# Optimization experiments

Hardware: AMD Instinct MI355X
Metric: run time of the kernel (lower is better)

The kernel has to match this reference:

```python
import jax, jax.numpy as jnp
import numpy as np

B, T, D = 2, 1024, 2048
H, HKV, DH = 16, 4, 128
G = H // HKV  # GQA groups
F = 5632
ROPE_THETA = 10000.0
EPS = 1e-6


def _rope_tables(t, dh, theta):
    inv = 1.0 / (theta ** (np.arange(0, dh, 2, dtype=np.float32) / dh))  # [dh//2]
    ang = np.outer(np.arange(t, dtype=np.float32), inv)                  # [T, dh//2]
    return jnp.asarray(np.cos(ang)), jnp.asarray(np.sin(ang))


def setup_inputs() -> dict:
    key = jax.random.key(0)
    ks = jax.random.split(key, 9)
    s = 0.02
    cos, sin = _rope_tables(T, DH, ROPE_THETA)
    return {
        "x": jax.random.normal(ks[0], (B, T, D), jnp.float32),
        "freqs_cos": cos,
        "freqs_sin": sin,
        "w_norm1": jnp.ones((D,), jnp.float32),
        "w_norm2": jnp.ones((D,), jnp.float32),
        "wq": jax.random.normal(ks[1], (D, H * DH), jnp.float32) * s,
        "wk": jax.random.normal(ks[2], (D, HKV * DH), jnp.float32) * s,
        "wv": jax.random.normal(ks[3], (D, HKV * DH), jnp.float32) * s,
        "wo": jax.random.normal(ks[4], (D, D), jnp.float32) * s,
        "w1": jax.random.normal(ks[5], (D, F), jnp.float32) * s,
        "w2": jax.random.normal(ks[6], (F, D), jnp.float32) * s,
        "w3": jax.random.normal(ks[7], (D, F), jnp.float32) * s,
    }


def _rmsnorm(x, w):
    var = jnp.mean(jnp.square(x), axis=-1, keepdims=True)
    return x * jax.lax.rsqrt(var + EPS) * w


def _apply_rope(x, cos, sin):
    # x: [B, T, nH, DH]; cos/sin: [T, DH//2]
    xr = x.reshape(*x.shape[:-1], DH // 2, 2)
    x0, x1 = xr[..., 0], xr[..., 1]
    c = cos[None, :, None, :]
    s = sin[None, :, None, :]
    o0 = x0 * c - x1 * s
    o1 = x0 * s + x1 * c
    return jnp.stack([o0, o1], axis=-1).reshape(x.shape)


def reference(x, freqs_cos, freqs_sin, w_norm1, w_norm2, wq, wk, wv, wo, w1, w2, w3):
    residual = x
    xn = _rmsnorm(x, w_norm1)
    q = (xn @ wq).reshape(B, T, H, DH)
    k = (xn @ wk).reshape(B, T, HKV, DH)
    v = (xn @ wv).reshape(B, T, HKV, DH)
    q = _apply_rope(q, freqs_cos, freqs_sin)
    k = _apply_rope(k, freqs_cos, freqs_sin)
    # grouped heads: q -> [B, HKV, G, T, DH]; k,v -> [B, HKV, T, DH]
    q = q.transpose(0, 2, 1, 3).reshape(B, HKV, G, T, DH)
    k = k.transpose(0, 2, 1, 3)
    v = v.transpose(0, 2, 1, 3)
    scale = DH ** -0.5
    scores = jnp.einsum("bkgtd,bksd->bkgts", q, k) * scale  # [B,HKV,G,T,T]
    causal = jnp.tril(jnp.ones((T, T), dtype=bool))
    scores = jnp.where(causal, scores, -jnp.inf)
    attn = jax.nn.softmax(scores, axis=-1)
    out = jnp.einsum("bkgts,bksd->bkgtd", attn, v)  # [B,HKV,G,T,DH]
    out = out.reshape(B, H, T, DH).transpose(0, 2, 1, 3).reshape(B, T, D)
    x = residual + out @ wo
    h = _rmsnorm(x, w_norm2)
    ffn = (jax.nn.silu(h @ w1) * (h @ w3)) @ w2
    return x + ffn
```

## Files before the change

### kernel.cpp

```cpp
#include <hip/hip_runtime.h>
#include <hip/hip_bf16.h>
#include <math.h>

typedef __hip_bfloat16 bf16;
typedef __attribute__((ext_vector_type(8))) short bf16x8;
typedef __attribute__((ext_vector_type(4))) float f32x4;

__device__ __forceinline__ float b2f(bf16 v) { return __bfloat162float(v); }
__device__ __forceinline__ bf16  f2b(float v) { return __float2bfloat16(v); }

constexpr int Bc = 2, Tc = 1024, Dc = 2048, Hc = 16, HKVc = 4, DHc = 128, Fc = 5632;
constexpr int Mr = Bc * Tc;
constexpr int Nqkv = Hc * DHc + 2 * HKVc * DHc;

__device__ __forceinline__ void g2l16(void* lds, const void* g) {
  __builtin_amdgcn_global_load_lds(
      (const __attribute__((address_space(1))) unsigned int*)g,
      (__attribute__((address_space(3))) unsigned int*)lds, 16, 0, 0);
}

__global__ __launch_bounds__(256) void tcast_k(const float* __restrict__ src,
                                               bf16* __restrict__ dst,
                                               int N, int K) {
  __shared__ bf16 tile[64][68];
  const int t = threadIdx.x;
  const int n0 = blockIdx.x * 64, k0 = blockIdx.y * 64;
#pragma unroll
  for (int it = 0; it < 4; ++it) {
    const int kl = it * 16 + (t >> 4);
    const int nl = (t & 15) * 4;
    float4 v = *reinterpret_cast<const float4*>(src + (size_t)(k0 + kl) * N + n0 + nl);
    tile[kl][nl]     = f2b(v.x);
    tile[kl][nl + 1] = f2b(v.y);
    tile[kl][nl + 2] = f2b(v.z);
    tile[kl][nl + 3] = f2b(v.w);
  }
  __syncthreads();
  union { uint4 u; bf16 h[8]; } o;
#pragma unroll
  for (int it = 0; it < 2; ++it) {
    const int nl = it * 32 + (t >> 3);
    const int kl = (t & 7) * 8;
#pragma unroll
    for (int j = 0; j < 8; ++j) o.h[j] = tile[kl + j][nl];
    *reinterpret_cast<uint4*>(dst + (size_t)(n0 + nl) * K + k0 + kl) = o.u;
  }
}

__global__ __launch_bounds__(256) void tcast_ffn(const float* __restrict__ src,
                                                 bf16* __restrict__ dst,
                                                 int off) {
  __shared__ bf16 tile[64][68];
  const int t = threadIdx.x;
  const int n0 = blockIdx.x * 64, k0 = blockIdx.y * 64;
#pragma unroll
  for (int it = 0; it < 4; ++it) {
    const int kl = it * 16 + (t >> 4);
    const int nl = (t & 15) * 4;
    float4 v = *reinterpret_cast<const float4*>(src + (size_t)(k0 + kl) * Fc + n0 + nl);
    tile[kl][nl]     = f2b(v.x);
    tile[kl][nl + 1] = f2b(v.y);
    tile[kl][nl + 2] = f2b(v.z);
    tile[kl][nl + 3] = f2b(v.w);
  }
  __syncthreads();
  union { uint4 u; bf16 h[8]; } o;
#pragma unroll
  for (int it = 0; it < 2; ++it) {
    const int nl = it * 32 + (t >> 3);
    const int kl = (t & 7) * 8;
#pragma unroll
    for (int j = 0; j < 8; ++j) o.h[j] = tile[kl + j][nl];
    const int n = n0 + nl;
    const int r = ((n >> 4) << 5) + (n & 15) + off;
    *reinterpret_cast<uint4*>(dst + (size_t)r * Dc + k0 + kl) = o.u;
  }
}

__global__ __launch_bounds__(256) void rmsnorm_k(const float* __restrict__ x,
                                                 const float* __restrict__ w,
                                                 bf16* __restrict__ out) {
  const size_t rbase = (size_t)blockIdx.x * Dc;
  float ss = 0.f;
  for (int i = threadIdx.x; i < Dc; i += 256) {
    float v = x[rbase + i];
    ss += v * v;
  }
#pragma unroll
  for (int off = 32; off > 0; off >>= 1) ss += __shfl_down(ss, off, 64);
  __shared__ float red[4];
  const int lane = threadIdx.x & 63, wid = threadIdx.x >> 6;
  if (lane == 0) red[wid] = ss;
  __syncthreads();
  const float scale = rsqrtf((red[0] + red[1] + red[2] + red[3]) / (float)Dc + 1e-6f);
  for (int i = threadIdx.x; i < Dc; i += 256)
    out[rbase + i] = f2b(x[rbase + i] * scale * w[i]);
}

template <bool ADDRES>
__global__ __launch_bounds__(256) void gemm128(const bf16* __restrict__ A,
                                               const bf16* __restrict__ Bt,
                                               const float* __restrict__ Res,
                                               void* __restrict__ Out,
                                               int N, int K) {
  __shared__ __align__(16) bf16 As[128 * 32];
  __shared__ __align__(16) bf16 Bs[128 * 32];
  const int t = threadIdx.x;
  const int bm = blockIdx.y * 128, bn = blockIdx.x * 128;
  const int lane = t & 63, wv = t >> 6;
  const int wm = (wv & 1) * 64, wn = (wv >> 1) * 64;
  const int sr = t >> 2, sc = (t & 3) * 8;
  const bf16* ga = A + (size_t)(bm + sr) * K + sc;
  const bf16* gb = Bt + (size_t)(bn + sr) * K + sc;
  bf16* lA0 = As + sr * 32 + sc;
  bf16* lA1 = As + (64 + sr) * 32 + sc;
  bf16* lB0 = Bs + sr * 32 + sc;
  bf16* lB1 = Bs + (64 + sr) * 32 + sc;
  const size_t rstep = (size_t)64 * K;
  f32x4 acc[4][4] = {};
  const int fr = lane & 15, fko = (lane >> 4) * 8;
  for (int k0 = 0; k0 < K; k0 += 32) {
    __syncthreads();
    g2l16(lA0, ga + k0);
    g2l16(lA1, ga + rstep + k0);
    g2l16(lB0, gb + k0);
    g2l16(lB1, gb + rstep + k0);
    __syncthreads();
    bf16x8 af[4], bff[4];
#pragma unroll
    for (int i = 0; i < 4; ++i)
      af[i] = *reinterpret_cast<const bf16x8*>(As + (wm + i * 16 + fr) * 32 + fko);
#pragma unroll
    for (int j = 0; j < 4; ++j)
      bff[j] = *reinterpret_cast<const bf16x8*>(Bs + (wn + j * 16 + fr) * 32 + fko);
#pragma unroll
    for (int i = 0; i < 4; ++i)
#pragma unroll
      for (int j = 0; j < 4; ++j)
        acc[i][j] = __builtin_amdgcn_mfma_f32_16x16x32_bf16(af[i], bff[j], acc[i][j], 0, 0, 0);
  }
  const int er = (lane >> 4) * 4, ec = lane & 15;
#pragma unroll
  for (int i = 0; i < 4; ++i)
#pragma unroll
    for (int j = 0; j < 4; ++j) {
      const int row = bm + wm + i * 16 + er;
      const int col = bn + wn + j * 16 + ec;
#pragma unroll
      for (int r = 0; r < 4; ++r) {
        const size_t idx = (size_t)(row + r) * N + col;
        if (ADDRES) ((float*)Out)[idx] = Res[idx] + acc[i][j][r];
        else        ((bf16*)Out)[idx] = f2b(acc[i][j][r]);
      }
    }
}

template <int K>
__global__ __launch_bounds__(512, 2) void ffn_gemm256(const bf16* __restrict__ A,
                                                      const bf16* __restrict__ B,
                                                      bf16* __restrict__ act) {
  constexpr int NT = K / 64;
  constexpr int NIT = NT / 2;
  __shared__ bf16 As[2 * 256 * 64];
  __shared__ bf16 Bs[3 * 256 * 64];
  const int tid = threadIdx.x;
  const int lane = tid & 63, wv = tid >> 6;
  const int wr = wv >> 2, wc = wv & 3;
  const int fr = lane & 15, quad = lane >> 4;
  const int swz = fr & 7;
  const int bm = blockIdx.y * 256;
  const int bn = blockIdx.x * 256;
  const int lrow = tid >> 3;
  const int scol = ((tid & 7) ^ (lrow & 7)) * 8;
  const size_t rstep = (size_t)64 * K;

  auto stageA = [&](int t, int half) {
    const int buf = (t & 1) * 16384;
    const bf16* g = A + (size_t)(bm + half * 128 + lrow) * K + t * 64 + scol;
    bf16* d = As + buf + half * 8192 + (size_t)tid * 8;
    g2l16(d, g);
    g2l16(d + 4096, g + rstep);
  };
  auto stageB = [&](int t, int half, int buf) {
    const bf16* g = B + (size_t)(bn + half * 128 + lrow) * K + t * 64 + scol;
    bf16* d = Bs + buf * 16384 + half * 8192 + (size_t)tid * 8;
    g2l16(d, g);
    g2l16(d + 4096, g + rstep);
  };

  f32x4 acc[8][4] = {};
  const int u0 = (quad ^ swz) * 8;

  stageA(0, 0); stageA(0, 1);
  stageB(0, 0, 0); stageB(0, 1, 0);
  stageB(1, 0, 1); stageB(1, 1, 1);
  asm volatile("s_waitcnt vmcnt(4)" ::: "memory");
  __builtin_amdgcn_s_barrier();

  int rb0 = 0, rb1 = 1, sb = 2;
  for (int it = 0; it < NIT; ++it) {
    const int t1 = 2 * it + 1;
#pragma unroll
    for (int j = 0; j < 8; ++j) {
      const int bufT = (j < 4) ? 0 : 16384;
      const int bufB = ((j < 4) ? rb0 : rb1) * 16384;
      const int qr4 = ((j & 3) >> 1) * 4, qc2 = ((j & 3) & 1) * 2;
      bf16x8 af[4][2], bv[2][2];
      const bf16* Ab = As + bufT + (size_t)(wr * 128 + fr) * 64;
      const bf16* Bb = Bs + bufB + (size_t)(wc * 64 + fr) * 64;
#pragma unroll
      for (int ii = 0; ii < 4; ++ii) {
        af[ii][0] = *reinterpret_cast<const bf16x8*>(Ab + (qr4 + ii) * 1024 + u0);
        af[ii][1] = *reinterpret_cast<const bf16x8*>(Ab + (qr4 + ii) * 1024 + (u0 ^ 32));
      }
#pragma unroll
      for (int jj = 0; jj < 2; ++jj) {
        bv[jj][0] = *reinterpret_cast<const bf16x8*>(Bb + (qc2 + jj) * 1024 + u0);
        bv[jj][1] = *reinterpret_cast<const bf16x8*>(Bb + (qc2 + jj) * 1024 + (u0 ^ 32));
      }
      if (j == 0)      stageA(t1, 0);
      else if (j == 1) stageA(t1, 1);
      else if (j == 2) { if (2 * it + 2 < NT) stageB(2 * it + 2, 0, sb); }
      else if (j == 3) { if (2 * it + 2 < NT) stageB(2 * it + 2, 1, sb); }
      else if (j == 4) { if (2 * it + 2 < NT) stageA(2 * it + 2, 0); }
      else if (j == 5) { if (2 * it + 2 < NT) stageA(2 * it + 2, 1); }
      else if (j == 6) { if (2 * it + 3 < NT) stageB(2 * it + 3, 0, rb0); }
      else             { if (2 * it + 3 < NT) stageB(2 * it + 3, 1, rb0); }
      __builtin_amdgcn_s_barrier();
      asm volatile("s_waitcnt lgkmcnt(0)" ::: "memory");
      __builtin_amdgcn_sched_barrier(0);
      __builtin_amdgcn_s_setprio(1);
#pragma unroll
      for (int ii = 0; ii < 4; ++ii)
#pragma unroll
        for (int jj = 0; jj < 2; ++jj) {
          acc[qr4 + ii][qc2 + jj] = __builtin_amdgcn_mfma_f32_16x16x32_bf16(
              af[ii][0], bv[jj][0], acc[qr4 + ii][qc2 + jj], 0, 0, 0);
          acc[qr4 + ii][qc2 + jj] = __builtin_amdgcn_mfma_f32_16x16x32_bf16(
              af[ii][1], bv[jj][1], acc[qr4 + ii][qc2 + jj], 0, 0, 0);
        }
      __builtin_amdgcn_s_setprio(0);
      if (j == 3) {
        if (2 * it + 2 < NT) asm volatile("s_waitcnt vmcnt(4)" ::: "memory");
        else                 asm volatile("s_waitcnt vmcnt(0)" ::: "memory");
      } else if (j == 7) {
        if (2 * it + 3 < NT)      asm volatile("s_waitcnt vmcnt(4)" ::: "memory");
        else if (2 * it + 2 < NT) asm volatile("s_waitcnt vmcnt(0)" ::: "memory");
      }
      __builtin_amdgcn_s_barrier();
    }
    const int nrb0 = sb; sb = rb1; rb1 = rb0; rb0 = nrb0;
  }

  const int er = quad * 4, ec = lane & 15;
#pragma unroll
  for (int i = 0; i < 8; ++i) {
    const int row = bm + wr * 128 + i * 16 + er;
#pragma unroll
    for (int jp = 0; jp < 2; ++jp) {
      const f32x4 g = acc[i][2 * jp], u = acc[i][2 * jp + 1];
      const int f = blockIdx.x * 128 + wc * 32 + jp * 16 + ec;
#pragma unroll
      for (int r = 0; r < 4; ++r) {
        const float sg = g[r] / (1.f + __expf(-g[r]));
        act[(size_t)(row + r) * Fc + f] = f2b(sg * u[r]);
      }
    }
  }
}

__global__ __launch_bounds__(256) void repack_k(const bf16* __restrict__ qkv,
                                                const float* __restrict__ cosb,
                                                const float* __restrict__ sinb,
                                                bf16* __restrict__ Qr,
                                                bf16* __restrict__ Kr,
                                                bf16* __restrict__ Vt) {
  const int bt = blockIdx.x;
  const int b = bt >> 10, tp = bt & (Tc - 1);
  const int t0 = threadIdx.x;
  const bf16* row = qkv + (size_t)bt * Nqkv;
#pragma unroll
  for (int k = 0; k < 4; ++k) {
    int p2 = k * 256 + t0;
    int hh = p2 >> 6, i = p2 & 63;
    float c = cosb[tp * 64 + i], sn = sinb[tp * 64 + i];
    float x0 = b2f(row[hh * 128 + 2 * i]), x1 = b2f(row[hh * 128 + 2 * i + 1]);
    bf16* dst = Qr + ((size_t)(b * Hc + hh) * Tc + tp) * DHc + 2 * i;
    dst[0] = f2b(x0 * c - x1 * sn);
    dst[1] = f2b(x0 * sn + x1 * c);
  }
  {
    int hh = t0 >> 6, i = t0 & 63;
    float c = cosb[tp * 64 + i], sn = sinb[tp * 64 + i];
    float x0 = b2f(row[2048 + hh * 128 + 2 * i]), x1 = b2f(row[2048 + hh * 128 + 2 * i + 1]);
    bf16* dst = Kr + ((size_t)(b * HKVc + hh) * Tc + tp) * DHc + 2 * i;
    dst[0] = f2b(x0 * c - x1 * sn);
    dst[1] = f2b(x0 * sn + x1 * c);
  }
#pragma unroll
  for (int k = 0; k < 2; ++k) {
    int e = k * 256 + t0;
    int kvh = e >> 7, dd = e & 127;
    Vt[((size_t)(b * HKVc + kvh) * DHc + dd) * Tc + tp] = row[2560 + e];
  }
}

__global__ __launch_bounds__(256) void fattn(const bf16* __restrict__ Qr,
                                             const bf16* __restrict__ Kr,
                                             const bf16* __restrict__ Vt,
                                             bf16* __restrict__ ao) {
  __shared__ __align__(16) bf16 Ks[64 * 136];
  __shared__ __align__(16) bf16 Vts[128 * 72];
  __shared__ __align__(16) bf16 Ps[4][16 * 72];
  const int idx = blockIdx.x;
  const int r = idx & 15;
  const int qt = (r & 1) ? (15 - (r >> 1)) : (r >> 1);
  const int h = (idx >> 4) & 15;
  const int b = idx >> 8;
  const int kv = h >> 2;
  const int t = threadIdx.x, lane = t & 63, wv = t >> 6;
  const int fr = lane & 15, quad = lane >> 4;

  const bf16* Qbase = Qr + ((size_t)(b * Hc + h) * Tc + qt * 64) * DHc;
  const bf16* Kbase = Kr + (size_t)(b * HKVc + kv) * Tc * DHc;
  const bf16* Vbase = Vt + (size_t)(b * HKVc + kv) * DHc * Tc;

  bf16x8 qf[4];
#pragma unroll
  for (int c = 0; c < 4; ++c)
    qf[c] = *reinterpret_cast<const bf16x8*>(Qbase + (size_t)(wv * 16 + fr) * DHc + c * 32 + quad * 8);

  float m[4], l[4];
  f32x4 o[8] = {};
#pragma unroll
  for (int r2 = 0; r2 < 4; ++r2) { m[r2] = -3.0e38f; l[r2] = 0.f; }

  for (int kt = 0; kt <= qt; ++kt) {
    __syncthreads();
    {
      const bf16* src = Kbase + (size_t)kt * 64 * DHc;
#pragma unroll
      for (int i2 = 0; i2 < 4; ++i2) {
        int flat = i2 * 256 + t;
        int row = flat >> 4, c16 = flat & 15;
        uint4 v = *reinterpret_cast<const uint4*>(src + (size_t)row * DHc + c16 * 8);
        *reinterpret_cast<uint4*>(&Ks[row * 136 + c16 * 8]) = v;
      }
#pragma unroll
      for (int i2 = 0; i2 < 4; ++i2) {
        int flat = i2 * 256 + t;
        int row = flat >> 3, c8 = flat & 7;
        uint4 v = *reinterpret_cast<const uint4*>(Vbase + (size_t)row * Tc + kt * 64 + c8 * 8);
        *reinterpret_cast<uint4*>(&Vts[row * 72 + c8 * 8]) = v;
      }
    }
    __syncthreads();
    f32x4 s[4];
#pragma unroll
    for (int cb = 0; cb < 4; ++cb) {
      f32x4 acc = {};
#pragma unroll
      for (int kc = 0; kc < 4; ++kc) {
        bf16x8 kf = *reinterpret_cast<const bf16x8*>(&Ks[(cb * 16 + fr) * 136 + kc * 32 + quad * 8]);
        acc = __builtin_amdgcn_mfma_f32_16x16x32_bf16(qf[kc], kf, acc, 0, 0, 0);
      }
      s[cb] = acc * 0.08838834764831845f;
    }
    if (kt == qt) {
#pragma unroll
      for (int cb = 0; cb < 4; ++cb)
#pragma unroll
        for (int r2 = 0; r2 < 4; ++r2) {
          int key = cb * 16 + fr;
          int qg = wv * 16 + quad * 4 + r2;
          if (key > qg) s[cb][r2] = -3.0e38f;
        }
    }
    float tm[4], ts[4];
#pragma unroll
    for (int r2 = 0; r2 < 4; ++r2)
      tm[r2] = fmaxf(fmaxf(s[0][r2], s[1][r2]), fmaxf(s[2][r2], s[3][r2]));
#pragma unroll
    for (int off = 1; off < 16; off <<= 1)
#pragma unroll
      for (int r2 = 0; r2 < 4; ++r2)
        tm[r2] = fmaxf(tm[r2], __shfl_xor(tm[r2], off, 64));
    float al[4];
#pragma unroll
    for (int r2 = 0; r2 < 4; ++r2) {
      float mn = fmaxf(m[r2], tm[r2]);
      al[r2] = __expf(m[r2] - mn);
      m[r2] = mn;
      ts[r2] = 0.f;
    }
#pragma unroll
    for (int cb = 0; cb < 4; ++cb)
#pragma unroll
      for (int r2 = 0; r2 < 4; ++r2) {
        float e = __expf(s[cb][r2] - m[r2]);
        s[cb][r2] = e;
        ts[r2] += e;
      }
#pragma unroll
    for (int off = 1; off < 16; off <<= 1)
#pragma unroll
      for (int r2 = 0; r2 < 4; ++r2)
        ts[r2] += __shfl_xor(ts[r2], off, 64);
#pragma unroll
    for (int r2 = 0; r2 < 4; ++r2) l[r2] = l[r2] * al[r2] + ts[r2];
#pragma unroll
    for (int db = 0; db < 8; ++db)
#pragma unroll
      for (int r2 = 0; r2 < 4; ++r2) o[db][r2] *= al[r2];
    bf16* pw = Ps[wv];
#pragma unroll
    for (int cb = 0; cb < 4; ++cb)
#pragma unroll
      for (int r2 = 0; r2 < 4; ++r2)
        pw[(quad * 4 + r2) * 72 + cb * 16 + fr] = f2b(s[cb][r2]);
    bf16x8 pa[2];
    pa[0] = *reinterpret_cast<const bf16x8*>(&pw[fr * 72 + quad * 8]);
    pa[1] = *reinterpret_cast<const bf16x8*>(&pw[fr * 72 + 32 + quad * 8]);
#pragma unroll
    for (int db = 0; db < 8; ++db) {
      bf16x8 v0 = *reinterpret_cast<const bf16x8*>(&Vts[(db * 16 + fr) * 72 + quad * 8]);
      bf16x8 v1 = *reinterpret_cast<const bf16x8*>(&Vts[(db * 16 + fr) * 72 + 32 + quad * 8]);
      o[db] = __builtin_amdgcn_mfma_f32_16x16x32_bf16(pa[0], v0, o[db], 0, 0, 0);
      o[db] = __builtin_amdgcn_mfma_f32_16x16x32_bf16(pa[1], v1, o[db], 0, 0, 0);
    }
  }
#pragma unroll
  for (int r2 = 0; r2 < 4; ++r2) {
    float inv = 1.f / l[r2];
    int qg = qt * 64 + wv * 16 + quad * 4 + r2;
    bf16* orow = ao + (size_t)(b * Tc + qg) * Dc + h * DHc;
#pragma unroll
    for (int db = 0; db < 8; ++db)
      orow[db * 16 + fr] = f2b(o[db][r2] * inv);
  }
}

extern "C" void kernel_launch(void* const* d_in, const int* in_sizes, int n_in,
                              void* d_out, int out_size, void* d_ws, size_t ws_size,
                              hipStream_t stream) {
  const float* x    = (const float*)d_in[0];
  const float* fcos = (const float*)d_in[1];
  const float* fsin = (const float*)d_in[2];
  const float* wn1  = (const float*)d_in[3];
  const float* wn2  = (const float*)d_in[4];
  const float* wq   = (const float*)d_in[5];
  const float* wk   = (const float*)d_in[6];
  const float* wv   = (const float*)d_in[7];
  const float* wo   = (const float*)d_in[8];
  const float* w1   = (const float*)d_in[9];
  const float* w2   = (const float*)d_in[10];
  const float* w3   = (const float*)d_in[11];

  char* p = (char*)d_ws;
  bf16* wqkv_t = (bf16*)p;                 p += (size_t)Nqkv * Dc * 2;
  bf16* qkv    = (bf16*)p;                 p += (size_t)Mr * Nqkv * 2;
  float* xat   = (float*)d_ws;
  bf16* wo_t = (bf16*)p;                   p += (size_t)Dc * Dc * 2;
  bf16* w13t = (bf16*)p;                   p += (size_t)2 * Fc * Dc * 2;
  bf16* w2t  = w13t;
  bf16* xn   = (bf16*)p;                   p += (size_t)Mr * Dc * 2;
  bf16* ao   = (bf16*)p;                   p += (size_t)Mr * Dc * 2;
  bf16* act  = (bf16*)p;                   p += (size_t)Mr * Fc * 2;
  bf16* hb = xn;
  bf16* Qr = act;
  bf16* Kr = act + (size_t)Mr * Hc * DHc;
  bf16* Vtb = Kr + (size_t)Mr * HKVc * DHc;

  const dim3 blk(256);
  tcast_k<<<dim3(32, 32), blk, 0, stream>>>(wq, wqkv_t, 2048, 2048);
  tcast_k<<<dim3(8, 32), blk, 0, stream>>>(wk, wqkv_t + (size_t)2048 * 2048, 512, 2048);
  tcast_k<<<dim3(8, 32), blk, 0, stream>>>(wv, wqkv_t + (size_t)2560 * 2048, 512, 2048);
  tcast_k<<<dim3(32, 32), blk, 0, stream>>>(wo, wo_t, 2048, 2048);
  tcast_ffn<<<dim3(88, 32), blk, 0, stream>>>(w1, w13t, 0);
  tcast_ffn<<<dim3(88, 32), blk, 0, stream>>>(w3, w13t, 16);

  rmsnorm_k<<<Mr, blk, 0, stream>>>(x, wn1, xn);
  gemm128<false><<<dim3(Nqkv / 128, Mr / 128), blk, 0, stream>>>(xn, wqkv_t, nullptr, qkv, Nqkv, Dc);
  repack_k<<<Mr, blk, 0, stream>>>(qkv, fcos, fsin, Qr, Kr, Vtb);
  fattn<<<Bc * Hc * 16, blk, 0, stream>>>(Qr, Kr, Vtb, ao);
  gemm128<true><<<dim3(Dc / 128, Mr / 128), blk, 0, stream>>>(ao, wo_t, x, xat, Dc, Dc);
  rmsnorm_k<<<Mr, blk, 0, stream>>>(xat, wn2, hb);
  ffn_gemm256<Dc><<<dim3(2 * Fc / 256, Mr / 256), dim3(512), 0, stream>>>(hb, w13t, act);
  tcast_k<<<dim3(32, 88), blk, 0, stream>>>(w2, w2t, 2048, 5632);
  gemm128<true><<<dim3(Dc / 128, Mr / 128), blk, 0, stream>>>(act, w2t, xat, (float*)d_out, Dc, Fc);
}
```

Before: 645.1 us.

## Use split-K 256-tile GEMM with atomic accumulation for Wo and W2 projections

Replaces the 128-tile residual GEMMs for the output projection and the FFN down projection with a 256x256 tile, 512-thread kernel that splits K four ways and accumulates into an output prefilled with the residual via float atomics. A copy kernel seeds the output with the residual first. This is meant to raise the number of blocks for the small 2048x2048 outputs (64 tiles to 256 blocks) and use a deeper, more efficient pipelined MFMA loop. It adds an extra full-tensor copy, atomic traffic, and nondeterministic summation order.

New measurement: 653.2 us. No clear change (+1.3%).

```diff
diff --git a/kernel.cpp b/kernel.cpp
--- a/kernel.cpp
+++ b/kernel.cpp
@@ -75,6 +75,12 @@
     const int r = ((n >> 4) << 5) + (n & 15) + off;
     *reinterpret_cast<uint4*>(dst + (size_t)r * Dc + k0 + kl) = o.u;
   }
+}
+
+__global__ __launch_bounds__(256) void copy_f32(const float* __restrict__ src,
+                                                float* __restrict__ dst) {
+  const int i = blockIdx.x * 256 + threadIdx.x;
+  reinterpret_cast<float4*>(dst)[i] = reinterpret_cast<const float4*>(src)[i];
 }
 
 __global__ __launch_bounds__(256) void rmsnorm_k(const float* __restrict__ x,
@@ -269,6 +275,119 @@
   }
 }
 
+template <int KFULL, int KSUB>
+__global__ __launch_bounds__(512, 2) void gemm256sk(const bf16* __restrict__ A,
+                                                    const bf16* __restrict__ Bt,
+                                                    float* __restrict__ Out,
+                                                    int N) {
+  constexpr int NT = KSUB / 64;
+  constexpr int NIT = NT / 2;
+  __shared__ bf16 As[2 * 256 * 64];
+  __shared__ bf16 Bs[3 * 256 * 64];
+  const int tid = threadIdx.x;
+  const int lane = tid & 63, wv = tid >> 6;
+  const int wr = wv >> 2, wc = wv & 3;
+  const int fr = lane & 15, quad = lane >> 4;
+  const int swz = fr & 7;
+  const int bm = blockIdx.y * 256;
+  const int bn = blockIdx.x * 256;
+  const int kbase = blockIdx.z * KSUB;
+  const int lrow = tid >> 3;
+  const int scol = ((tid & 7) ^ (lrow & 7)) * 8;
+  const size_t rstep = (size_t)64 * KFULL;
+
+  auto stageA = [&](int t, int half) {
+    const int buf = (t & 1) * 16384;
+    const bf16* g = A + (size_t)(bm + half * 128 + lrow) * KFULL + kbase + t * 64 + scol;
+    bf16* d = As + buf + half * 8192 + (size_t)tid * 8;
+    g2l16(d, g);
+    g2l16(d + 4096, g + rstep);
+  };
+  auto stageB = [&](int t, int half, int buf) {
+    const bf16* g = Bt + (size_t)(bn + half * 128 + lrow) * KFULL + kbase + t * 64 + scol;
+    bf16* d = Bs + buf * 16384 + half * 8192 + (size_t)tid * 8;
+    g2l16(d, g);
+    g2l16(d + 4096, g + rstep);
+  };
+
+  f32x4 acc[8][4] = {};
+  const int u0 = (quad ^ swz) * 8;
+
+  stageA(0, 0); stageA(0, 1);
+  stageB(0, 0, 0); stageB(0, 1, 0);
+  stageB(1, 0, 1); stageB(1, 1, 1);
+  asm volatile("s_waitcnt vmcnt(4)" ::: "memory");
+  __builtin_amdgcn_s_barrier();
+
+  int rb0 = 0, rb1 = 1, sb = 2;
+  for (int it = 0; it < NIT; ++it) {
+    const int t1 = 2 * it + 1;
+#pragma unroll
+    for (int j = 0; j < 8; ++j) {
+      const int bufT = (j < 4) ? 0 : 16384;
+      const int bufB = ((j < 4) ? rb0 : rb1) * 16384;
+      const int qr4 = ((j & 3) >> 1) * 4, qc2 = ((j & 3) & 1) * 2;
+      bf16x8 af[4][2], bv[2][2];
+      const bf16* Ab = As + bufT + (size_t)(wr * 128 + fr) * 64;
+      const bf16* Bb = Bs + bufB + (size_t)(wc * 64 + fr) * 64;
+#pragma unroll
+      for (int ii = 0; ii < 4; ++ii) {
+        af[ii][0] = *reinterpret_cast<const bf16x8*>(Ab + (qr4 + ii) * 1024 + u0);
+        af[ii][1] = *reinterpret_cast<const bf16x8*>(Ab + (qr4 + ii) * 1024 + (u0 ^ 32));
+      }
+#pragma unroll
+      for (int jj = 0; jj < 2; ++jj) {
+        bv[jj][0] = *reinterpret_cast<const bf16x8*>(Bb + (qc2 + jj) * 1024 + u0);
+        bv[jj][1] = *reinterpret_cast<const bf16x8*>(Bb + (qc2 + jj) * 1024 + (u0 ^ 32));
+      }
+      if (j == 0)      stageA(t1, 0);
+      else if (j == 1) stageA(t1, 1);
+      else if (j == 2) { if (2 * it + 2 < NT) stageB(2 * it + 2, 0, sb); }
+      else if (j == 3) { if (2 * it + 2 < NT) stageB(2 * it + 2, 1, sb); }
+      else if (j == 4) { if (2 * it + 2 < NT) stageA(2 * it + 2, 0); }
+      else if (j == 5) { if (2 * it + 2 < NT) stageA(2 * it + 2, 1); }
+      else if (j == 6) { if (2 * it + 3 < NT) stageB(2 * it + 3, 0, rb0); }
+      else             { if (2 * it + 3 < NT) stageB(2 * it + 3, 1, rb0); }
+      __builtin_amdgcn_s_barrier();
+      asm volatile("s_waitcnt lgkmcnt(0)" ::: "memory");
+      __builtin_amdgcn_sched_barrier(0);
+      __builtin_amdgcn_s_setprio(1);
+#pragma unroll
+      for (int ii = 0; ii < 4; ++ii)
+#pragma unroll
+        for (int jj = 0; jj < 2; ++jj) {
+          acc[qr4 + ii][qc2 + jj] = __builtin_amdgcn_mfma_f32_16x16x32_bf16(
+              af[ii][0], bv[jj][0], acc[qr4 + ii][qc2 + jj], 0, 0, 0);
+          acc[qr4 + ii][qc2 + jj] = __builtin_amdgcn_mfma_f32_16x16x32_bf16(
+              af[ii][1], bv[jj][1], acc[qr4 + ii][qc2 + jj], 0, 0, 0);
+        }
+      __builtin_amdgcn_s_setprio(0);
+      if (j == 3) {
+        if (2 * it + 2 < NT) asm volatile("s_waitcnt vmcnt(4)" ::: "memory");
+        else                 asm volatile("s_waitcnt vmcnt(0)" ::: "memory");
+      } else if (j == 7) {
+        if (2 * it + 3 < NT)      asm volatile("s_waitcnt vmcnt(4)" ::: "memory");
+        else if (2 * it + 2 < NT) asm volatile("s_waitcnt vmcnt(0)" ::: "memory");
+      }
+      __builtin_amdgcn_s_barrier();
+    }
+    const int nrb0 = sb; sb = rb1; rb1 = rb0; rb0 = nrb0;
+  }
+
+  const int er = quad * 4, ec = lane & 15;
+#pragma unroll
+  for (int i = 0; i < 8; ++i) {
+    const int row = bm + wr * 128 + i * 16 + er;
+#pragma unroll
+    for (int jc = 0; jc < 4; ++jc) {
+      const int col = bn + wc * 64 + jc * 16 + ec;
+#pragma unroll
+      for (int r = 0; r < 4; ++r)
+        atomicAdd(&Out[(size_t)(row + r) * N + col], acc[i][jc][r]);
+    }
+  }
+}
+
 __global__ __launch_bounds__(256) void repack_k(const bf16* __restrict__ qkv,
                                                 const float* __restrict__ cosb,
                                                 const float* __restrict__ sinb,
@@ -483,9 +602,11 @@
   gemm128<false><<<dim3(Nqkv / 128, Mr / 128), blk, 0, stream>>>(xn, wqkv_t, nullptr, qkv, Nqkv, Dc);
   repack_k<<<Mr, blk, 0, stream>>>(qkv, fcos, fsin, Qr, Kr, Vtb);
   fattn<<<Bc * Hc * 16, blk, 0, stream>>>(Qr, Kr, Vtb, ao);
-  gemm128<true><<<dim3(Dc / 128, Mr / 128), blk, 0, stream>>>(ao, wo_t, x, xat, Dc, Dc);
+  copy_f32<<<Mr * Dc / 1024, blk, 0, stream>>>(x, xat);
+  gemm256sk<Dc, 512><<<dim3(Dc / 256, Mr / 256, 4), dim3(512), 0, stream>>>(ao, wo_t, xat, Dc);
   rmsnorm_k<<<Mr, blk, 0, stream>>>(xat, wn2, hb);
   ffn_gemm256<Dc><<<dim3(2 * Fc / 256, Mr / 256), dim3(512), 0, stream>>>(hb, w13t, act);
   tcast_k<<<dim3(32, 88), blk, 0, stream>>>(w2, w2t, 2048, 5632);
-  gemm128<true><<<dim3(Dc / 128, Mr / 128), blk, 0, stream>>>(act, w2t, xat, (float*)d_out, Dc, Fc);
-}
+  copy_f32<<<Mr * Dc / 1024, blk, 0, stream>>>(xat, (float*)d_out);
+  gemm256sk<Fc, 1408><<<dim3(Dc / 256, Mr / 256, 4), dim3(512), 0, stream>>>(act, w2t, (float*)d_out, Dc);
+}
```
